# Kernel optimization log

Hardware: AMD Instinct MI355X
Metric: run time of the kernel (lower is better)

The kernel has to match this reference:

```python
import jax, jax.numpy as jnp
import numpy as np

COMMITMENT_COST = 0.25

def _conv(x, w, stride, pad):
    return jax.lax.conv_general_dilated(
        x, w, window_strides=(stride, stride),
        padding=((pad, pad), (pad, pad)),
        dimension_numbers=("NCHW", "OIHW", "NCHW"))

def _gelu(x):
    return jax.nn.gelu(x, approximate=False)

def setup_inputs() -> dict:
    key = jax.random.key(0)
    ks = jax.random.split(key, 9)
    def w(k, shape):
        fan_in = shape[1] * shape[2] * shape[3]
        return jax.random.normal(k, shape, jnp.float32) / jnp.sqrt(fan_in)
    return {
        "x": jax.random.normal(ks[0], (32, 3, 256, 256), jnp.float32),
        "enc_w1": w(ks[1], (64, 3, 5, 5)),
        "enc_w2": w(ks[2], (64, 64, 5, 5)),
        "enc_w3": w(ks[3], (64, 64, 2, 2)),
        "dec_w1": w(ks[4], (512, 64, 2, 2)),
        "dec_w2": w(ks[5], (256, 512, 2, 2)),
        "dec_w3": w(ks[6], (256, 256, 2, 2)),
        "codes": jax.random.normal(ks[7], (24, 64), jnp.float32),
        "ema_count": jax.random.uniform(ks[8], (24,), jnp.float32) + 0.1,
    }

def reference(x, enc_w1, enc_w2, enc_w3, dec_w1, dec_w2, dec_w3, codes, ema_count):
    # ---- encoder: 256 -> 128 -> 64 -> 63, channels 3 -> 64 ----
    z = _conv(x, enc_w1, 2, 2)
    z = _gelu(z)
    z = _conv(z, enc_w2, 2, 2)
    z = _gelu(z)
    z = _conv(z, enc_w3, 1, 0)          # [B, 64, 63, 63]

    # ---- VQ codebook (EMA variant: commitment loss only) ----
    B, C, H, W = z.shape
    zf = jnp.transpose(z, (0, 2, 3, 1)).reshape(-1, C)          # [N, C]
    # squared L2 distances to each code
    d = (jnp.sum(zf * zf, axis=1, keepdims=True)
         - 2.0 * zf @ codes.T
         + jnp.sum(codes * codes, axis=1))                       # [N, K]
    idx = jnp.argmin(d, axis=1)                                  # [N]
    zq = codes[idx].reshape(B, H, W, C).transpose(0, 3, 1, 2)    # [B, C, H, W]

    vq_loss = COMMITMENT_COST * jnp.mean(
        (jax.lax.stop_gradient(zq) - z) ** 2)
    # straight-through estimator
    z_hat = z + jax.lax.stop_gradient(zq - z)

    # code probabilities from EMA cluster counts, gathered per position
    probs = ema_count / jnp.sum(ema_count)                       # [K]
    z_probs = probs[idx].reshape(B, H, W)                        # [B, H, W]

    # ---- decoder: 63 -> 64 -> 63 -> 64, channels 64 -> 512 -> 256 -> 256 ----
    y = _conv(z_hat, dec_w1, 1, 1)
    y = _gelu(y)
    y = _conv(y, dec_w2, 1, 0)
    y = _gelu(y)
    x_hat = _conv(y, dec_w3, 1, 1)      # [B, 256, 64, 64]

    return (x_hat, z_probs, vq_loss)
```

## Files before the change

### kernel.cpp

```cpp
#include <hip/hip_runtime.h>
#include <hip/hip_bf16.h>


#define DEV_INLINE __device__ __forceinline__

typedef __attribute__((ext_vector_type(8))) short bf16x8;
typedef __attribute__((ext_vector_type(4))) float f32x4;

#define GLL16(g, l) __builtin_amdgcn_global_load_lds(                      \
    (const __attribute__((address_space(1))) void*)(g),                    \
    (__attribute__((address_space(3))) void*)(l), 16, 0, 0)

DEV_INLINE float gelu_exact(float v) {
    return 0.5f * v * (1.0f + erff(v * 0.70710678118654752440f));
}

__global__ void wtf_k(const float* __restrict__ w, float* __restrict__ wt,
                      int C, int total) {
    int t = blockIdx.x * 256 + threadIdx.x;
    if (t >= total) return;
    int oc = t & 63;
    int rest = t >> 6;
    int tap = rest % 25, c = rest / 25;
    wt[t] = w[(oc * C + c) * 25 + tap];
}

template<int C, int IH, int IW>
__global__ __launch_bounds__(256) void conv5s2_t(
    const float* __restrict__ xg,
    const float* __restrict__ wt,
    float* __restrict__ outg) {
    constexpr int OH = IH / 2, OW = IW / 2;
    __shared__ float xin[35 * 36];
    __shared__ float wl[1600];
    const int tid = threadIdx.x;
    const int n = blockIdx.z;
    const int OY0 = blockIdx.y * 16, OX0 = blockIdx.x * 16;
    const int IY0 = OY0 * 2 - 2, IX0 = OX0 * 2 - 2;
    const int og = tid & 3;
    const int pg = tid >> 2;
    const int py = (pg >> 3) * 2, px = (pg & 7) * 2;
    const int ry = py * 2, rx = px * 2;

    f32x4 a00 = {0,0,0,0}, a01 = a00, a02 = a00, a03 = a00;
    f32x4 a10 = a00, a11 = a00, a12 = a00, a13 = a00;
    f32x4 a20 = a00, a21 = a00, a22 = a00, a23 = a00;
    f32x4 a30 = a00, a31 = a00, a32 = a00, a33 = a00;

    const float* xn = xg + (size_t)n * C * IH * IW;
    for (int c = 0; c < C; ++c) {
        {
            const float4* wsrc = (const float4*)(wt + c * 1600);
            float4* wdst = (float4*)wl;
            wdst[tid] = wsrc[tid];
            if (tid < 144) wdst[256 + tid] = wsrc[256 + tid];
        }
        const float* zc = xn + (size_t)c * IH * IW;
        for (int i = tid; i < 1225; i += 256) {
            int r = i / 35, cl = i - r * 35;
            int iy = IY0 + r, ix = IX0 + cl;
            float v = 0.f;
            if ((unsigned)iy < (unsigned)IH && (unsigned)ix < (unsigned)IW)
                v = zc[(size_t)iy * IW + ix];
            xin[r * 36 + cl] = v;
        }
        __syncthreads();
#pragma unroll
        for (int ky = 0; ky < 5; ++ky) {
            const float* r0 = xin + (ry + ky) * 36 + rx;
            const float* r1 = r0 + 72;
#pragma unroll
            for (int kx = 0; kx < 5; ++kx) {
                const f32x4* wq = (const f32x4*)(wl + (ky * 5 + kx) * 64 + og * 16);
                f32x4 w0 = wq[0], w1 = wq[1], w2 = wq[2], w3 = wq[3];
                float xA = r0[kx], xB = r0[kx + 2];
                float xC = r1[kx], xD = r1[kx + 2];
                a00 += xA * w0; a01 += xA * w1; a02 += xA * w2; a03 += xA * w3;
                a10 += xB * w0; a11 += xB * w1; a12 += xB * w2; a13 += xB * w3;
                a20 += xC * w0; a21 += xC * w1; a22 += xC * w2; a23 += xC * w3;
                a30 += xD * w0; a31 += xD * w1; a32 += xD * w2; a33 += xD * w3;
            }
        }
        __syncthreads();
    }
    const int ocb = og * 16;
#define CSTORE(v, oy, ox, q) {                                                \
        float* o = outg + (((size_t)n * 64 + ocb + (q) * 4) * OH + (oy)) * OW \
                   + (ox);                                                    \
        o[0]               = gelu_exact((v).x);                               \
        o[(size_t)OH * OW]     = gelu_exact((v).y);                           \
        o[(size_t)2 * OH * OW] = gelu_exact((v).z);                           \
        o[(size_t)3 * OH * OW] = gelu_exact((v).w); }
    CSTORE(a00, OY0 + py,     OX0 + px,     0); CSTORE(a01, OY0 + py,     OX0 + px,     1);
    CSTORE(a02, OY0 + py,     OX0 + px,     2); CSTORE(a03, OY0 + py,     OX0 + px,     3);
    CSTORE(a10, OY0 + py,     OX0 + px + 1, 0); CSTORE(a11, OY0 + py,     OX0 + px + 1, 1);
    CSTORE(a12, OY0 + py,     OX0 + px + 1, 2); CSTORE(a13, OY0 + py,     OX0 + px + 1, 3);
    CSTORE(a20, OY0 + py + 1, OX0 + px,     0); CSTORE(a21, OY0 + py + 1, OX0 + px,     1);
    CSTORE(a22, OY0 + py + 1, OX0 + px,     2); CSTORE(a23, OY0 + py + 1, OX0 + px,     3);
    CSTORE(a30, OY0 + py + 1, OX0 + px + 1, 0); CSTORE(a31, OY0 + py + 1, OX0 + px + 1, 1);
    CSTORE(a32, OY0 + py + 1, OX0 + px + 1, 2); CSTORE(a33, OY0 + py + 1, OX0 + px + 1, 3);
#undef CSTORE
}

__global__ void conv3_k(const float* __restrict__ z2,
                        const float* __restrict__ w,
                        float* __restrict__ z) {
    __shared__ float wl[1024];
    const int oc0 = blockIdx.y * 4;
    for (int i = threadIdx.x; i < 1024; i += 256) {
        int j = i & 3, r = i >> 2;
        wl[i] = w[(oc0 + j) * 256 + r];
    }
    __syncthreads();
    const int s = blockIdx.x * 256 + threadIdx.x;
    if (s >= 3969) return;
    const int n = blockIdx.z;
    const int oy = s / 63, ox = s % 63;
    const float4* wv = (const float4*)wl;
    float a0 = 0.f, a1 = 0.f, a2 = 0.f, a3 = 0.f;
    const float* zn = z2 + n * 64 * 4096;
    for (int c = 0; c < 64; ++c) {
        const float* zc = zn + c * 4096;
#pragma unroll
        for (int tap = 0; tap < 4; ++tap) {
            int iy = oy + (tap >> 1), ix = ox + (tap & 1);
            float xv = zc[iy * 64 + ix];
            float4 wq = wv[c * 4 + tap];
            a0 += xv * wq.x; a1 += xv * wq.y; a2 += xv * wq.z; a3 += xv * wq.w;
        }
    }
    int obase = (n * 64 + oc0) * 3969 + s;
    z[obase]            = a0;
    z[obase + 3969]     = a1;
    z[obase + 2 * 3969] = a2;
    z[obase + 3 * 3969] = a3;
}

__global__ void vq_k(const float* __restrict__ z,
                     const float* __restrict__ codes,
                     const float* __restrict__ ema,
                     int* __restrict__ idxO,
                     float* __restrict__ zprobsO,
                     float* __restrict__ lossO) {
    __shared__ float cl[1536];
    __shared__ float cn[24];
    __shared__ float pr[24];
    for (int i = threadIdx.x; i < 1536; i += 256) cl[i] = codes[i];
    if (threadIdx.x < 24) pr[threadIdx.x] = ema[threadIdx.x];
    __syncthreads();
    if (threadIdx.x < 24) {
        float sm = 0.f;
        for (int c = 0; c < 64; ++c) { float v = cl[threadIdx.x * 64 + c]; sm += v * v; }
        cn[threadIdx.x] = sm;
    }
    __syncthreads();
    int t = blockIdx.x * 256 + threadIdx.x;
    float l = 0.f;
    if (t < 127008) {
        int b = t / 3969, s = t - b * 3969;
        const float* zp = z + (b * 64) * 3969 + s;
        float zv[64];
        float zn = 0.f;
#pragma unroll
        for (int c = 0; c < 64; ++c) { float v = zp[c * 3969]; zv[c] = v; zn += v * v; }
        float best = 1e30f; int bi = 0;
        for (int k = 0; k < 24; ++k) {
            float dot = 0.f;
#pragma unroll
            for (int c = 0; c < 64; ++c) dot += zv[c] * cl[k * 64 + c];
            float d = zn - 2.f * dot + cn[k];
            if (d < best) { best = d; bi = k; }
        }
        idxO[t] = bi;
        float psum = 0.f;
        for (int k = 0; k < 24; ++k) psum += pr[k];
        zprobsO[t] = pr[bi] / psum;
        for (int c = 0; c < 64; ++c) { float dd = cl[bi * 64 + c] - zv[c]; l += dd * dd; }
    }
    for (int off = 32; off; off >>= 1) l += __shfl_down(l, off, 64);
    if ((threadIdx.x & 63) == 0) atomicAdd(lossO, l);
}

__global__ void dtab_k(const float* __restrict__ codes,
                       const float* __restrict__ w1,
                       float* __restrict__ D) {
    int t = blockIdx.x * 256 + threadIdx.x;
    if (t >= 24 * 4 * 512) return;
    int oc = t & 511, tap = (t >> 9) & 3, k = t >> 11;
    float acc = 0.f;
    for (int c = 0; c < 64; ++c)
        acc += codes[k * 64 + c] * w1[oc * 256 + c * 4 + tap];
    D[t] = acc;
}

__global__ void wt_k(const float* __restrict__ w, __hip_bfloat16* __restrict__ wT,
                     int cl2, int total) {
    int t = blockIdx.x * 256 + threadIdx.x;
    if (t >= total) return;
    int c = t & ((1 << cl2) - 1);
    int tap = (t >> cl2) & 3;
    int oc = t >> (cl2 + 2);
    wT[t] = __float2bfloat16(w[((oc << cl2) + c) * 4 + tap]);
}

__global__ void dec1_k(const int* __restrict__ idx,
                       const float* __restrict__ D,
                       __hip_bfloat16* __restrict__ y1) {
    const int pos = blockIdx.x;
    const int n = pos >> 12, rem = pos & 4095;
    const int iy = rem >> 6, ix = rem & 63;
    const int* idn = idx + n * 3969;
    const int t = threadIdx.x;
    float ax = 0.f, ay = 0.f;
#pragma unroll
    for (int tap = 0; tap < 4; ++tap) {
        int py = iy - 1 + (tap >> 1), px = ix - 1 + (tap & 1);
        if ((unsigned)py < 63u && (unsigned)px < 63u) {
            int k = idn[py * 63 + px];
            float2 v = ((const float2*)(D + (k * 4 + tap) * 512))[t];
            ax += v.x; ay += v.y;
        }
    }
    __hip_bfloat162 o;
    o.x = __float2bfloat16(gelu_exact(ax));
    o.y = __float2bfloat16(gelu_exact(ay));
    ((__hip_bfloat162*)(y1 + (size_t)pos * 512))[t] = o;
}

__global__ __launch_bounds__(256) void dec2_mfma(
    const __hip_bfloat16* __restrict__ y1,
    const __hip_bfloat16* __restrict__ wT,
    const __hip_bfloat16* __restrict__ zp,
    __hip_bfloat16* __restrict__ y2)
{
    __shared__ __hip_bfloat16 As[128 * 32];
    __shared__ __hip_bfloat16 Bs[128 * 32];
    const int tid = threadIdx.x;
    const int wave = tid >> 6, lane = tid & 63;
    const int quad = lane >> 4, l15 = lane & 15;
    const int m0 = blockIdx.x * 128;
    const int oc0 = blockIdx.y * 128;
    const int sub = tid & 3;

    const char* pA[2];
    const char* pB[2];
#pragma unroll
    for (int j = 0; j < 2; ++j) {
        int slot = j * 64 + (tid >> 2);
        int pp = m0 + slot;
        if (pp < 127008) {
            int n = pp / 3969; int r = pp - n * 3969;
            int oy = r / 63;  int ox = r - oy * 63;
            pA[j] = (const char*)y1 + (size_t)((n * 64 + oy) * 64 + ox) * 1024 + sub * 16;
        } else {
            pA[j] = (const char*)zp;
        }
        pB[j] = (const char*)wT + (size_t)(oc0 + slot) * 4096 + sub * 16;
    }
    char* ldsA[2] = {(char*)As + wave * 1024, (char*)As + 4096 + wave * 1024};
    char* ldsB[2] = {(char*)Bs + wave * 1024, (char*)Bs + 4096 + wave * 1024};

    f32x4 acc[4][4] = {};
    const int wm = (wave & 1) * 64;
    const int wn = (wave >> 1) * 64;

#pragma unroll
    for (int tap = 0; tap < 4; ++tap) {
        const int toff = ((tap >> 1) * 64 + (tap & 1)) * 1024;
        for (int kk = 0; kk < 16; ++kk) {
            const int cb = kk * 64;
            GLL16(pA[0] + toff + cb, ldsA[0]);
            GLL16(pA[1] + toff + cb, ldsA[1]);
            GLL16(pB[0] + tap * 1024 + cb, ldsB[0]);
            GLL16(pB[1] + tap * 1024 + cb, ldsB[1]);
            __syncthreads();
            bf16x8 af[4], bf[4];
#pragma unroll
            for (int mi = 0; mi < 4; ++mi)
                af[mi] = *(const bf16x8*)((const char*)As + (wm + mi * 16 + l15) * 64 + quad * 16);
#pragma unroll
            for (int ni = 0; ni < 4; ++ni)
                bf[ni] = *(const bf16x8*)((const char*)Bs + (wn + ni * 16 + l15) * 64 + quad * 16);
#pragma unroll
            for (int mi = 0; mi < 4; ++mi)
#pragma unroll
                for (int ni = 0; ni < 4; ++ni)
                    acc[mi][ni] = __builtin_amdgcn_mfma_f32_16x16x32_bf16(
                        af[mi], bf[ni], acc[mi][ni], 0, 0, 0);
            __syncthreads();
        }
    }
#pragma unroll
    for (int mi = 0; mi < 4; ++mi)
#pragma unroll
        for (int r = 0; r < 4; ++r) {
            int pos = m0 + wm + mi * 16 + quad * 4 + r;
            if (pos < 127008) {
#pragma unroll
                for (int ni = 0; ni < 4; ++ni) {
                    int oc = oc0 + wn + ni * 16 + l15;
                    y2[(size_t)pos * 256 + oc] =
                        __float2bfloat16(gelu_exact(acc[mi][ni][r]));
                }
            }
        }
}

__global__ __launch_bounds__(256) void dec3_mfma(
    const __hip_bfloat16* __restrict__ y2,
    const __hip_bfloat16* __restrict__ wT,
    const __hip_bfloat16* __restrict__ zp,
    float* __restrict__ out)
{
    __shared__ __hip_bfloat16 As[128 * 32];
    __shared__ __hip_bfloat16 Bs[128 * 32];
    const int tid = threadIdx.x;
    const int wave = tid >> 6, lane = tid & 63;
    const int quad = lane >> 4, l15 = lane & 15;
    const int p0 = blockIdx.x * 128;
    const int oc0 = blockIdx.y * 128;
    const int sub = tid & 3;

    const char* pW[2];
    const char* pP[4][2];
#pragma unroll
    for (int j = 0; j < 2; ++j) {
        int slot = j * 64 + (tid >> 2);
        pW[j] = (const char*)wT + (size_t)(oc0 + slot) * 2048 + sub * 16;
        int pp = p0 + slot;
        int n = pp >> 12, rem = pp & 4095;
        int OY = rem >> 6, OX = rem & 63;
#pragma unroll
        for (int tap = 0; tap < 4; ++tap) {
            int iy = OY - 1 + (tap >> 1), ix = OX - 1 + (tap & 1);
            if ((unsigned)iy < 63u && (unsigned)ix < 63u)
                pP[tap][j] = (const char*)y2 + (size_t)(n * 3969 + iy * 63 + ix) * 512 + sub * 16;
            else
                pP[tap][j] = (const char*)zp;
        }
    }
    char* ldsA[2] = {(char*)As + wave * 1024, (char*)As + 4096 + wave * 1024};
    char* ldsB[2] = {(char*)Bs + wave * 1024, (char*)Bs + 4096 + wave * 1024};

    f32x4 acc[4][4] = {};
    const int wm = (wave & 1) * 64;
    const int wn = (wave >> 1) * 64;

#pragma unroll
    for (int tap = 0; tap < 4; ++tap) {
        for (int kk = 0; kk < 8; ++kk) {
            const int cb = kk * 64;
            GLL16(pW[0] + tap * 512 + cb, ldsA[0]);
            GLL16(pW[1] + tap * 512 + cb, ldsA[1]);
            GLL16(pP[tap][0] + cb, ldsB[0]);
            GLL16(pP[tap][1] + cb, ldsB[1]);
            __syncthreads();
            bf16x8 af[4], bf[4];
#pragma unroll
            for (int mi = 0; mi < 4; ++mi)
                af[mi] = *(const bf16x8*)((const char*)As + (wm + mi * 16 + l15) * 64 + quad * 16);
#pragma unroll
            for (int ni = 0; ni < 4; ++ni)
                bf[ni] = *(const bf16x8*)((const char*)Bs + (wn + ni * 16 + l15) * 64 + quad * 16);
#pragma unroll
            for (int mi = 0; mi < 4; ++mi)
#pragma unroll
                for (int ni = 0; ni < 4; ++ni)
                    acc[mi][ni] = __builtin_amdgcn_mfma_f32_16x16x32_bf16(
                        af[mi], bf[ni], acc[mi][ni], 0, 0, 0);
            __syncthreads();
        }
    }
    const int n = p0 >> 12;
    const int posLocal0 = (p0 & 4095) + wn;
#pragma unroll
    for (int mi = 0; mi < 4; ++mi)
#pragma unroll
        for (int r = 0; r < 4; ++r) {
            int oc = oc0 + wm + mi * 16 + quad * 4 + r;
            float* orow = out + ((size_t)(n * 256 + oc) << 12);
#pragma unroll
            for (int ni = 0; ni < 4; ++ni)
                orow[posLocal0 + ni * 16 + l15] = acc[mi][ni][r];
        }
}

__global__ void loss_k(const float* __restrict__ lossO, float* __restrict__ out) {
    out[0] = 0.25f * lossO[0] / 8128512.0f;
}

extern "C" void kernel_launch(void* const* d_in, const int* in_sizes, int n_in,
                              void* d_out, int out_size, void* d_ws, size_t ws_size,
                              hipStream_t stream) {
    const float* x     = (const float*)d_in[0];
    const float* ew1   = (const float*)d_in[1];
    const float* ew2   = (const float*)d_in[2];
    const float* ew3   = (const float*)d_in[3];
    const float* dw1   = (const float*)d_in[4];
    const float* dw2   = (const float*)d_in[5];
    const float* dw3   = (const float*)d_in[6];
    const float* codes = (const float*)d_in[7];
    const float* ema   = (const float*)d_in[8];
    float* out = (float*)d_out;

    char* ws = (char*)d_ws;
    float* z1   = (float*)(ws + 0);
    float* z2   = (float*)(ws + 134217728);
    float* z    = (float*)(ws + 167772160);
    int*   idx  = (int*)  (ws + 200286208);
    float* loss = (float*)(ws + 200794240);
    __hip_bfloat16* zp  = (__hip_bfloat16*)(ws + 200794496);
    float* D    = (float*)(ws + 200864128);
    __hip_bfloat16* wT2 = (__hip_bfloat16*)(ws + 201650560);
    __hip_bfloat16* wT3 = (__hip_bfloat16*)(ws + 202699136);
    float* wt2f = (float*)(ws + 201650560);
    float* wt1f = (float*)(ws + 202699136);
    __hip_bfloat16* y1  = (__hip_bfloat16*)(ws + 0);
    __hip_bfloat16* y2  = (__hip_bfloat16*)(ws + 134217728);

    hipMemsetAsync(loss, 0, 4, stream);
    hipMemsetAsync(zp, 0, 69632, stream);

    wtf_k<<<dim3(19), 256, 0, stream>>>(ew1, wt1f, 3, 4800);
    wtf_k<<<dim3(400), 256, 0, stream>>>(ew2, wt2f, 64, 102400);
    conv5s2_t<3, 256, 256><<<dim3(8, 8, 32), 256, 0, stream>>>(x, wt1f, z1);
    conv5s2_t<64, 128, 128><<<dim3(4, 4, 32), 256, 0, stream>>>(z1, wt2f, z2);
    conv3_k<<<dim3(16, 16, 32), 256, 0, stream>>>(z2, ew3, z);
    vq_k<<<dim3(497), 256, 0, stream>>>(z, codes, ema, idx, out + 33554432, loss);
    dtab_k<<<dim3(192), 256, 0, stream>>>(codes, dw1, D);
    wt_k<<<dim3(2048), 256, 0, stream>>>(dw2, wT2, 9, 524288);
    wt_k<<<dim3(1024), 256, 0, stream>>>(dw3, wT3, 8, 262144);
    dec1_k<<<dim3(131072), 256, 0, stream>>>(idx, D, y1);
    dec2_mfma<<<dim3(993, 2), 256, 0, stream>>>(y1, wT2, zp, y2);
    dec3_mfma<<<dim3(1024, 2), 256, 0, stream>>>(y2, wT3, zp, out);
    loss_k<<<1, 1, 0, stream>>>(loss, out + 33681440);
}
```

Before: 1.230 ms.

## Double-buffer encoder conv input tiles and read wave-uniform weights from global

```diff
diff --git a/kernel.cpp b/kernel.cpp
--- a/kernel.cpp
+++ b/kernel.cpp
@@ -26,80 +26,121 @@
 }
 
 template<int C, int IH, int IW>
-__global__ __launch_bounds__(256) void conv5s2_t(
+__global__ __launch_bounds__(256) void conv5s2_s(
     const float* __restrict__ xg,
     const float* __restrict__ wt,
     float* __restrict__ outg) {
     constexpr int OH = IH / 2, OW = IW / 2;
-    __shared__ float xin[35 * 36];
-    __shared__ float wl[1600];
+    __shared__ float xin[2][35 * 36];
     const int tid = threadIdx.x;
+    const int lane = tid & 63;
+    const int og = __builtin_amdgcn_readfirstlane(tid >> 6);
     const int n = blockIdx.z;
     const int OY0 = blockIdx.y * 16, OX0 = blockIdx.x * 16;
     const int IY0 = OY0 * 2 - 2, IX0 = OX0 * 2 - 2;
-    const int og = tid & 3;
-    const int pg = tid >> 2;
-    const int py = (pg >> 3) * 2, px = (pg & 7) * 2;
+    const int py = lane >> 2;
+    const int px = (lane & 3) * 4;
     const int ry = py * 2, rx = px * 2;
+
+    const bool interior = (IY0 >= 0) && (IY0 + 35 <= IH) &&
+                          (IX0 >= 0) && (IX0 + 36 <= IW);
+
+    const int s0 = tid;
+    const int s1 = 256 + tid;
+    const bool has1 = (tid < 59);
+    const int r0 = s0 / 9, q0 = s0 - r0 * 9;
+    const int r1 = s1 / 9, q1 = s1 - r1 * 9;
+
+    const float* xn = xg + (size_t)n * C * IH * IW;
+
+    auto LD = [&](const float* zc, int r, int q, bool active) -> f32x4 {
+        f32x4 v = {0.f, 0.f, 0.f, 0.f};
+        if (active) {
+            int iy = IY0 + r, ixb = IX0 + q * 4;
+            if (interior) {
+                const float2* p = (const float2*)(zc + (size_t)iy * IW + ixb);
+                float2 a = p[0], b = p[1];
+                v[0] = a.x; v[1] = a.y; v[2] = b.x; v[3] = b.y;
+            } else if ((unsigned)iy < (unsigned)IH) {
+#pragma unroll
+                for (int j = 0; j < 4; ++j) {
+                    int ix = ixb + j;
+                    if ((unsigned)ix < (unsigned)IW)
+                        v[j] = zc[(size_t)iy * IW + ix];
+                }
+            }
+        }
+        return v;
+    };
+
+    {
+        f32x4 pA = LD(xn, r0, q0, true);
+        f32x4 pB = LD(xn, r1, q1, has1);
+        *(f32x4*)(&xin[0][0] + s0 * 4) = pA;
+        if (has1) *(f32x4*)(&xin[0][0] + s1 * 4) = pB;
+    }
+    __syncthreads();
 
     f32x4 a00 = {0,0,0,0}, a01 = a00, a02 = a00, a03 = a00;
     f32x4 a10 = a00, a11 = a00, a12 = a00, a13 = a00;
     f32x4 a20 = a00, a21 = a00, a22 = a00, a23 = a00;
     f32x4 a30 = a00, a31 = a00, a32 = a00, a33 = a00;
 
-    const float* xn = xg + (size_t)n * C * IH * IW;
+#define XEL(i) ((i) < 4 ? A0[(i) & 3] : ((i) < 8 ? A1[(i) & 3] : A2[(i) & 3]))
+
     for (int c = 0; c < C; ++c) {
-        {
-            const float4* wsrc = (const float4*)(wt + c * 1600);
-            float4* wdst = (float4*)wl;
-            wdst[tid] = wsrc[tid];
-            if (tid < 144) wdst[256 + tid] = wsrc[256 + tid];
-        }
-        const float* zc = xn + (size_t)c * IH * IW;
-        for (int i = tid; i < 1225; i += 256) {
-            int r = i / 35, cl = i - r * 35;
-            int iy = IY0 + r, ix = IX0 + cl;
-            float v = 0.f;
-            if ((unsigned)iy < (unsigned)IH && (unsigned)ix < (unsigned)IW)
-                v = zc[(size_t)iy * IW + ix];
-            xin[r * 36 + cl] = v;
-        }
-        __syncthreads();
+        const int buf = c & 1;
+        f32x4 sA, sB;
+        const bool more = (c + 1 < C);
+        if (more) {
+            const float* zc = xn + (size_t)(c + 1) * IH * IW;
+            sA = LD(zc, r0, q0, true);
+            sB = LD(zc, r1, q1, has1);
+        }
+        const float* xb = &xin[buf][0];
+        const float* wc = wt + (size_t)c * 1600 + og * 16;
 #pragma unroll
         for (int ky = 0; ky < 5; ++ky) {
-            const float* r0 = xin + (ry + ky) * 36 + rx;
-            const float* r1 = r0 + 72;
+            const f32x4* xr = (const f32x4*)(xb + (ry + ky) * 36 + rx);
+            f32x4 A0 = xr[0], A1 = xr[1], A2 = xr[2];
 #pragma unroll
             for (int kx = 0; kx < 5; ++kx) {
-                const f32x4* wq = (const f32x4*)(wl + (ky * 5 + kx) * 64 + og * 16);
+                const f32x4* wq = (const f32x4*)(wc + (ky * 5 + kx) * 64);
                 f32x4 w0 = wq[0], w1 = wq[1], w2 = wq[2], w3 = wq[3];
-                float xA = r0[kx], xB = r0[kx + 2];
-                float xC = r1[kx], xD = r1[kx + 2];
+                float xA = XEL(kx),     xB = XEL(kx + 2);
+                float xC = XEL(kx + 4), xD = XEL(kx + 6);
                 a00 += xA * w0; a01 += xA * w1; a02 += xA * w2; a03 += xA * w3;
                 a10 += xB * w0; a11 += xB * w1; a12 += xB * w2; a13 += xB * w3;
                 a20 += xC * w0; a21 += xC * w1; a22 += xC * w2; a23 += xC * w3;
                 a30 += xD * w0; a31 += xD * w1; a32 += xD * w2; a33 += xD * w3;
             }
         }
+        if (more) {
+            float* xw = &xin[buf ^ 1][0];
+            *(f32x4*)(xw + s0 * 4) = sA;
+            if (has1) *(f32x4*)(xw + s1 * 4) = sB;
+        }
         __syncthreads();
     }
-    const int ocb = og * 16;
-#define CSTORE(v, oy, ox, q) {                                                \
-        float* o = outg + (((size_t)n * 64 + ocb + (q) * 4) * OH + (oy)) * OW \
-                   + (ox);                                                    \
-        o[0]               = gelu_exact((v).x);                               \
-        o[(size_t)OH * OW]     = gelu_exact((v).y);                           \
-        o[(size_t)2 * OH * OW] = gelu_exact((v).z);                           \
-        o[(size_t)3 * OH * OW] = gelu_exact((v).w); }
-    CSTORE(a00, OY0 + py,     OX0 + px,     0); CSTORE(a01, OY0 + py,     OX0 + px,     1);
-    CSTORE(a02, OY0 + py,     OX0 + px,     2); CSTORE(a03, OY0 + py,     OX0 + px,     3);
-    CSTORE(a10, OY0 + py,     OX0 + px + 1, 0); CSTORE(a11, OY0 + py,     OX0 + px + 1, 1);
-    CSTORE(a12, OY0 + py,     OX0 + px + 1, 2); CSTORE(a13, OY0 + py,     OX0 + px + 1, 3);
-    CSTORE(a20, OY0 + py + 1, OX0 + px,     0); CSTORE(a21, OY0 + py + 1, OX0 + px,     1);
-    CSTORE(a22, OY0 + py + 1, OX0 + px,     2); CSTORE(a23, OY0 + py + 1, OX0 + px,     3);
-    CSTORE(a30, OY0 + py + 1, OX0 + px + 1, 0); CSTORE(a31, OY0 + py + 1, OX0 + px + 1, 1);
-    CSTORE(a32, OY0 + py + 1, OX0 + px + 1, 2); CSTORE(a33, OY0 + py + 1, OX0 + px + 1, 3);
-#undef CSTORE
+#undef XEL
+
+    const size_t HW = (size_t)OH * OW;
+    float* ob = outg + ((size_t)n * 64 + og * 16) * HW
+                + (size_t)(OY0 + py) * OW + (OX0 + px);
+#define STQ(qi, v0, v1, v2, v3) {                                          \
+        float* o = ob + (size_t)(qi) * 4 * HW;                             \
+        _Pragma("unroll")                                                  \
+        for (int j = 0; j < 4; ++j) {                                      \
+            f32x4 t;                                                       \
+            t[0] = gelu_exact((v0)[j]); t[1] = gelu_exact((v1)[j]);        \
+            t[2] = gelu_exact((v2)[j]); t[3] = gelu_exact((v3)[j]);        \
+            *(f32x4*)(o + (size_t)j * HW) = t;                             \
+        } }
+    STQ(0, a00, a10, a20, a30)
+    STQ(1, a01, a11, a21, a31)
+    STQ(2, a02, a12, a22, a32)
+    STQ(3, a03, a13, a23, a33)
+#undef STQ
 }
 
 __global__ void conv3_k(const float* __restrict__ z2,
@@ -423,8 +464,8 @@
 
     wtf_k<<<dim3(19), 256, 0, stream>>>(ew1, wt1f, 3, 4800);
     wtf_k<<<dim3(400), 256, 0, stream>>>(ew2, wt2f, 64, 102400);
-    conv5s2_t<3, 256, 256><<<dim3(8, 8, 32), 256, 0, stream>>>(x, wt1f, z1);
-    conv5s2_t<64, 128, 128><<<dim3(4, 4, 32), 256, 0, stream>>>(z1, wt2f, z2);
+    conv5s2_s<3, 256, 256><<<dim3(8, 8, 32), 256, 0, stream>>>(x, wt1f, z1);
+    conv5s2_s<64, 128, 128><<<dim3(4, 4, 32), 256, 0, stream>>>(z1, wt2f, z2);
     conv3_k<<<dim3(16, 16, 32), 256, 0, stream>>>(z2, ew3, z);
     vq_k<<<dim3(497), 256, 0, stream>>>(z, codes, ema, idx, out + 33554432, loss);
     dtab_k<<<dim3(192), 256, 0, stream>>>(codes, dw1, D);
```

After: 1.398 ms. 1.14x slower.

## Replace second encoder conv with register-tiled 16x16 output kernel

Applied to the files above, without the earlier changes.

```diff
diff --git a/kernel.cpp b/kernel.cpp
--- a/kernel.cpp
+++ b/kernel.cpp
@@ -102,6 +102,90 @@
 #undef CSTORE
 }
 
+template<int C, int IH, int IW>
+__global__ __launch_bounds__(256) void conv5s2_r(
+    const float* __restrict__ xg,
+    const float* __restrict__ wt,
+    float* __restrict__ outg) {
+    constexpr int OH = IH / 2, OW = IW / 2;
+    __shared__ float xin[35 * 36];
+    __shared__ float wl[1600];
+    const int tid = threadIdx.x;
+    const int n = blockIdx.z;
+    const int OY0 = blockIdx.y * 16, OX0 = blockIdx.x * 16;
+    const int IY0 = OY0 * 2 - 2, IX0 = OX0 * 2 - 2;
+    const int og = tid & 7;
+    const int pg = tid >> 3;
+    const int py = (pg >> 2) * 2, px = (pg & 3) * 4;
+    const int ry = py * 2, rx = px * 2;
+
+    f32x4 a000 = {0,0,0,0}, a001 = a000, a010 = a000, a011 = a000;
+    f32x4 a020 = a000, a021 = a000, a030 = a000, a031 = a000;
+    f32x4 a100 = a000, a101 = a000, a110 = a000, a111 = a000;
+    f32x4 a120 = a000, a121 = a000, a130 = a000, a131 = a000;
+
+    const float* xn = xg + (size_t)n * C * IH * IW;
+    for (int c = 0; c < C; ++c) {
+        {
+            const float4* wsrc = (const float4*)(wt + c * 1600);
+            float4* wdst = (float4*)wl;
+            wdst[tid] = wsrc[tid];
+            if (tid < 144) wdst[256 + tid] = wsrc[256 + tid];
+        }
+        const float* zc = xn + (size_t)c * IH * IW;
+        for (int i = tid; i < 1225; i += 256) {
+            int r = i / 35, cl = i - r * 35;
+            int iy = IY0 + r, ix = IX0 + cl;
+            float v = 0.f;
+            if ((unsigned)iy < (unsigned)IH && (unsigned)ix < (unsigned)IW)
+                v = zc[(size_t)iy * IW + ix];
+            xin[r * 36 + cl] = v;
+        }
+        __syncthreads();
+#pragma unroll
+        for (int ky = 0; ky < 5; ++ky) {
+            const float* r0 = xin + (ry + ky) * 36 + rx;
+            const float* r1 = r0 + 72;
+#pragma unroll
+            for (int kx = 0; kx < 5; ++kx) {
+                const f32x4* wq = (const f32x4*)(wl + (ky * 5 + kx) * 64 + og * 8);
+                f32x4 w0 = wq[0], w1 = wq[1];
+                float xA = r0[kx],     xB = r0[kx + 2];
+                float xC = r0[kx + 4], xD = r0[kx + 6];
+                float xE = r1[kx],     xF = r1[kx + 2];
+                float xG = r1[kx + 4], xH = r1[kx + 6];
+                a000 += xA * w0; a001 += xA * w1;
+                a010 += xB * w0; a011 += xB * w1;
+                a020 += xC * w0; a021 += xC * w1;
+                a030 += xD * w0; a031 += xD * w1;
+                a100 += xE * w0; a101 += xE * w1;
+                a110 += xF * w0; a111 += xF * w1;
+                a120 += xG * w0; a121 += xG * w1;
+                a130 += xH * w0; a131 += xH * w1;
+            }
+        }
+        __syncthreads();
+    }
+
+    const size_t HW = (size_t)OH * OW;
+#define STR(q, vA, vB, vC, vD, vE, vF, vG, vH) {                           \
+        _Pragma("unroll")                                                  \
+        for (int j = 0; j < 4; ++j) {                                      \
+            float* o = outg + ((size_t)n * 64 + og * 8 + (q) * 4 + j) * HW \
+                       + (size_t)(OY0 + py) * OW + (OX0 + px);             \
+            f32x4 t0, t1;                                                  \
+            t0[0] = gelu_exact((vA)[j]); t0[1] = gelu_exact((vB)[j]);      \
+            t0[2] = gelu_exact((vC)[j]); t0[3] = gelu_exact((vD)[j]);      \
+            t1[0] = gelu_exact((vE)[j]); t1[1] = gelu_exact((vF)[j]);      \
+            t1[2] = gelu_exact((vG)[j]); t1[3] = gelu_exact((vH)[j]);      \
+            *(f32x4*)o = t0;                                               \
+            *(f32x4*)(o + OW) = t1;                                        \
+        } }
+    STR(0, a000, a010, a020, a030, a100, a110, a120, a130)
+    STR(1, a001, a011, a021, a031, a101, a111, a121, a131)
+#undef STR
+}
+
 __global__ void conv3_k(const float* __restrict__ z2,
                         const float* __restrict__ w,
                         float* __restrict__ z) {
@@ -424,7 +508,7 @@
     wtf_k<<<dim3(19), 256, 0, stream>>>(ew1, wt1f, 3, 4800);
     wtf_k<<<dim3(400), 256, 0, stream>>>(ew2, wt2f, 64, 102400);
     conv5s2_t<3, 256, 256><<<dim3(8, 8, 32), 256, 0, stream>>>(x, wt1f, z1);
-    conv5s2_t<64, 128, 128><<<dim3(4, 4, 32), 256, 0, stream>>>(z1, wt2f, z2);
+    conv5s2_r<64, 128, 128><<<dim3(4, 4, 32), 256, 0, stream>>>(z1, wt2f, z2);
     conv3_k<<<dim3(16, 16, 32), 256, 0, stream>>>(z2, ew3, z);
     vq_k<<<dim3(497), 256, 0, stream>>>(z, codes, ema, idx, out + 33554432, loss);
     dtab_k<<<dim3(192), 256, 0, stream>>>(codes, dw1, D);
```

Result: no change. 1.208 ms (-1.8%).

## Add smaller-tile parity-split LDS conv kernel for second encoder conv

Applied to the files above, without the earlier changes.

```diff
diff --git a/kernel.cpp b/kernel.cpp
--- a/kernel.cpp
+++ b/kernel.cpp
@@ -102,6 +102,105 @@
 #undef CSTORE
 }
 
+template<int C, int IH, int IW>
+__global__ __launch_bounds__(256, 4) void conv5s2_g(
+    const float* __restrict__ xg,
+    const float* __restrict__ wt,
+    float* __restrict__ outg) {
+    constexpr int OH = IH / 2, OW = IW / 2;
+    __shared__ float xp[760];
+    const int tid = threadIdx.x;
+    const int n = blockIdx.z;
+    const int OY0 = blockIdx.y * 8, OX0 = blockIdx.x * 16;
+    const int IY0 = OY0 * 2 - 2, IX0 = OX0 * 2 - 2;
+    const int og = tid & 15;
+    const int pg = tid >> 4;
+    const int py = (pg >> 2) * 2;
+    const int px = (pg & 3) * 4;
+    const int ry = py * 2;
+
+    int  sG[3]; int sL[3]; bool sIn[3]; bool sWr[3];
+#pragma unroll
+    for (int k = 0; k < 3; ++k) {
+        int s = tid + k * 256;
+        int r = s / 36, cl = s - r * 36;
+        int iy = IY0 + r, ix = IX0 + cl;
+        sWr[k] = (s < 684);
+        sIn[k] = sWr[k] && ((unsigned)iy < (unsigned)IH) &&
+                 ((unsigned)ix < (unsigned)IW);
+        sG[k] = sIn[k] ? (iy * IW + ix) : 0;
+        sL[k] = sWr[k] ? ((cl & 1) * 380 + r * 20 + (cl >> 1)) : 0;
+    }
+
+    const float* xn = xg + (size_t)n * C * IH * IW;
+    const float* wtb = wt + og * 4;
+
+    f32x4 a00 = {0,0,0,0}, a01 = a00, a02 = a00, a03 = a00;
+    f32x4 a10 = a00, a11 = a00, a12 = a00, a13 = a00;
+
+    for (int c = 0; c < C; ++c) {
+        const float* zc = xn + (size_t)c * IH * IW;
+#pragma unroll
+        for (int k = 0; k < 3; ++k) {
+            if (sWr[k]) {
+                float v = sIn[k] ? zc[sG[k]] : 0.f;
+                xp[sL[k]] = v;
+            }
+        }
+        __syncthreads();
+
+        const float* wc = wtb + (size_t)c * 1600;
+#define PICK8(Qa, Qb, i) ((i) < 4 ? (Qa)[(i) & 3] : (Qb)[(i) & 3])
+#define XV(R, kx, jj) (((kx) & 1)                                           \
+        ? PICK8(O##R##0, O##R##1, (jj) + ((kx) >> 1))                       \
+        : PICK8(E##R##0, E##R##1, (jj) + ((kx) >> 1)))
+#pragma unroll
+        for (int ky = 0; ky < 5; ++ky) {
+            f32x4 w0 = *(const f32x4*)(wc + (ky * 5 + 0) * 64);
+            f32x4 w1 = *(const f32x4*)(wc + (ky * 5 + 1) * 64);
+            f32x4 w2 = *(const f32x4*)(wc + (ky * 5 + 2) * 64);
+            f32x4 w3 = *(const f32x4*)(wc + (ky * 5 + 3) * 64);
+            f32x4 w4 = *(const f32x4*)(wc + (ky * 5 + 4) * 64);
+            const float* e0 = xp + (ry + ky) * 20 + px;
+            const float* o0 = e0 + 380;
+            const float* e1 = e0 + 40;
+            const float* o1 = o0 + 40;
+            const f32x4 E00 = *(const f32x4*)e0, E01 = *(const f32x4*)(e0 + 4);
+            const f32x4 O00 = *(const f32x4*)o0, O01 = *(const f32x4*)(o0 + 4);
+            const f32x4 E10 = *(const f32x4*)e1, E11 = *(const f32x4*)(e1 + 4);
+            const f32x4 O10 = *(const f32x4*)o1, O11 = *(const f32x4*)(o1 + 4);
+#pragma unroll
+            for (int kx = 0; kx < 5; ++kx) {
+                const f32x4 wv = (kx == 0) ? w0 : (kx == 1) ? w1
+                               : (kx == 2) ? w2 : (kx == 3) ? w3 : w4;
+                float xA = XV(0, kx, 0), xB = XV(0, kx, 1);
+                float xC = XV(0, kx, 2), xD = XV(0, kx, 3);
+                float xE = XV(1, kx, 0), xF = XV(1, kx, 1);
+                float xG = XV(1, kx, 2), xH = XV(1, kx, 3);
+                a00 += xA * wv; a01 += xB * wv; a02 += xC * wv; a03 += xD * wv;
+                a10 += xE * wv; a11 += xF * wv; a12 += xG * wv; a13 += xH * wv;
+            }
+        }
+#undef XV
+#undef PICK8
+        __syncthreads();
+    }
+
+    const size_t HW = (size_t)OH * OW;
+#pragma unroll
+    for (int j = 0; j < 4; ++j) {
+        float* o = outg + ((size_t)n * 64 + og * 4 + j) * HW
+                   + (size_t)(OY0 + py) * OW + (OX0 + px);
+        f32x4 t0, t1;
+        t0[0] = gelu_exact(a00[j]); t0[1] = gelu_exact(a01[j]);
+        t0[2] = gelu_exact(a02[j]); t0[3] = gelu_exact(a03[j]);
+        t1[0] = gelu_exact(a10[j]); t1[1] = gelu_exact(a11[j]);
+        t1[2] = gelu_exact(a12[j]); t1[3] = gelu_exact(a13[j]);
+        *(f32x4*)o = t0;
+        *(f32x4*)(o + OW) = t1;
+    }
+}
+
 __global__ void conv3_k(const float* __restrict__ z2,
                         const float* __restrict__ w,
                         float* __restrict__ z) {
@@ -424,7 +523,7 @@
     wtf_k<<<dim3(19), 256, 0, stream>>>(ew1, wt1f, 3, 4800);
     wtf_k<<<dim3(400), 256, 0, stream>>>(ew2, wt2f, 64, 102400);
     conv5s2_t<3, 256, 256><<<dim3(8, 8, 32), 256, 0, stream>>>(x, wt1f, z1);
-    conv5s2_t<64, 128, 128><<<dim3(4, 4, 32), 256, 0, stream>>>(z1, wt2f, z2);
+    conv5s2_g<64, 128, 128><<<dim3(4, 8, 32), 256, 0, stream>>>(z1, wt2f, z2);
     conv3_k<<<dim3(16, 16, 32), 256, 0, stream>>>(z2, ew3, z);
     vq_k<<<dim3(497), 256, 0, stream>>>(z, codes, ema, idx, out + 33554432, loss);
     dtab_k<<<dim3(192), 256, 0, stream>>>(codes, dw1, D);
```

Result: faster. 1.198 ms (-2.6%).
